# Optimization experiments

Hardware: AMD Instinct MI355X
Metric: run time of the kernel (lower is better)

Reference implementation:

```python
import jax, jax.numpy as jnp
import numpy as np

B, LQ, LK = 32, 2048, 2048
D_IN = 32   # vk_i_dim == q_i_dim == v_dim
D_KQ = 20   # kq_dim
EPS = 1e-5

def _layernorm(x, g, b):
    m = jnp.mean(x, axis=-1, keepdims=True)
    v = jnp.mean(jnp.square(x - m), axis=-1, keepdims=True)
    return (x - m) * jax.lax.rsqrt(v + EPS) * g + b

def setup_inputs() -> dict:
    key = jax.random.key(0)
    ks = jax.random.split(key, 8)
    s_in = 1.0 / np.sqrt(D_IN)
    return {
        "vals": jax.random.normal(ks[0], (B, LK, D_IN), jnp.float32),
        "keys": jax.random.normal(ks[1], (B, LK, D_IN), jnp.float32),
        "ques": jax.random.normal(ks[2], (B, LQ, D_IN), jnp.float32),
        "key_mask": jax.random.randint(ks[3], (B, LK), 0, 2) == 1,
        # Linear weights stored torch-style [out, in]; applied as x @ W.T
        "W_v": jax.random.uniform(ks[4], (D_IN, D_IN), jnp.float32, -s_in, s_in),
        "W_k": jax.random.uniform(ks[5], (D_KQ, D_IN), jnp.float32, -s_in, s_in),
        "W_q": jax.random.uniform(ks[6], (D_KQ, D_IN), jnp.float32, -s_in, s_in),
        "g_k": jnp.ones((D_KQ,), jnp.float32),
        "b_k": jnp.zeros((D_KQ,), jnp.float32),
        "g_q": jnp.ones((D_KQ,), jnp.float32),
        "b_q": jnp.zeros((D_KQ,), jnp.float32),
        "g_o": jnp.ones((D_IN,), jnp.float32),
        "b_o": jnp.zeros((D_IN,), jnp.float32),
    }

def reference(vals, keys, ques, key_mask, W_v, W_k, W_q, g_k, b_k, g_q, b_q, g_o, b_o):
    # v = linear_v(vals); k = LN(linear_k(keys)); q = LN(linear_q(ques))
    v = jnp.einsum('bkd,vd->bkv', vals, W_v)                    # [B,LK,32]
    k = _layernorm(jnp.einsum('bkd,cd->bkc', keys, W_k), g_k, b_k)  # [B,LK,20]
    q = _layernorm(jnp.einsum('bqd,cd->bqc', ques, W_q), g_q, b_q)  # [B,LQ,20]
    scale = jnp.asarray(D_KQ, jnp.float32) ** 0.5
    a = jnp.einsum('bqc,bkc->bqk', q, k) / scale                # [B,LQ,LK]
    a = jnp.where(key_mask[:, None, :], -jnp.inf, a)
    p = jax.nn.softmax(a, axis=-1)
    # dropout(p=0.1) in eval mode is identity
    o = jnp.einsum('bqk,bkv->bqv', p, v)                        # [B,LQ,32]
    return _layernorm(o + ques, g_o, b_o)
```

## Files before the change

kernel.cpp:

```cpp
#include <hip/hip_runtime.h>

#define NB   32
#define LQ   2048
#define LK   2048
#define EPSF 1e-5f
#define SCALE_L2E 0.32260327f
#define C_L2E     7.2134752f

#define MASK_I32  0
#define MASK_B8   1
#define MASK_BF16 2
#define MASK_F32  3

typedef __attribute__((ext_vector_type(8))) short  short8;
typedef __attribute__((ext_vector_type(4))) float  floatx4;

__device__ __forceinline__ unsigned short f2b(float f) {
    union { float f; unsigned int i; } c; c.f = f;
    unsigned int x = c.i;
    return (unsigned short)((x + 0x7FFFu + ((x >> 16) & 1u)) >> 16);
}

__device__ __forceinline__ int mask_nz(const void* m, int g, int enc) {
    switch (enc) {
        case MASK_B8:   return ((const unsigned char*)m)[g]  != 0;
        case MASK_BF16: return ((const unsigned short*)m)[g] != 0;
        case MASK_F32:  return ((const unsigned int*)m)[g]   != 0;
        default:        return ((const int*)m)[g]            != 0;
    }
}

__global__ __launch_bounds__(256) void proj_kv_kernel(
    const float4* __restrict__ vals,
    const float4* __restrict__ keys,
    const void*   __restrict__ key_mask,
    const float4* __restrict__ Wv,
    const float4* __restrict__ Wk,
    const float*  __restrict__ gk,
    const float*  __restrict__ bk,
    int*            __restrict__ counts,
    unsigned short* __restrict__ kbf,
    unsigned short* __restrict__ vTb)
{
    __shared__ float smem[1704];
    __shared__ int sc[3];
    float* sWv = smem;
    float* sWk = smem + 1024;
    float* sgk = smem + 1664;
    float* sbk = smem + 1684;
    const int tid = threadIdx.x;
    if (tid < 3) sc[tid] = 0;
    __syncthreads();

    ((float4*)sWv)[tid] = Wv[tid];
    if (tid < 160) ((float4*)sWk)[tid] = Wk[tid];
    if (tid < 20) sgk[tid] = gk[tid];
    if (tid >= 32 && tid < 52) sbk[tid - 32] = bk[tid - 32];
    {
        const unsigned char* mbytes = (const unsigned char*)key_mask;
        int l0 = 0, l1 = 0, l2 = 0;
        for (int i = tid; i < 1024; i += 256) {
            const unsigned char mb = mbytes[i];
            if ((i & 3) == 1 && mb == 0x3Fu) l0++;
            if ((i & 3) == 3 && mb == 0x3Fu) l1++;
            if ((i & 1) == 1 && mb == 0x01u) l2++;
        }
        if (l0) atomicAdd(&sc[0], l0);
        if (l1) atomicAdd(&sc[1], l1);
        if (l2) atomicAdd(&sc[2], l2);
    }
    __syncthreads();
    const int enc = sc[0] ? MASK_BF16 : (sc[1] ? MASK_F32 : (sc[2] ? MASK_B8 : MASK_I32));

    const int g = blockIdx.x * 256 + tid;
    const int b = g >> 11;
    const int lane = tid & 63;

    const int valid = mask_nz(key_mask, g, enc) ? 0 : 1;
    const unsigned long long mb = __ballot(valid);
    const int cnt = __popcll(mb);
    int base = 0;
    if (lane == 0) base = atomicAdd(&counts[b], cnt);
    base = __shfl(base, 0);
    const int slot = base + __popcll(mb & ((1ull << lane) - 1ull));

    float x[32];

    {
        const float4* kp = keys + (size_t)g * 8;
        #pragma unroll
        for (int t = 0; t < 8; ++t) {
            float4 u = kp[t];
            x[t*4+0] = u.x; x[t*4+1] = u.y; x[t*4+2] = u.z; x[t*4+3] = u.w;
        }
        const float4* wk4 = (const float4*)sWk;
        float kv[20];
        #pragma unroll
        for (int c = 0; c < 20; ++c) {
            float s = 0.f;
            #pragma unroll
            for (int i = 0; i < 8; ++i) {
                float4 ww = wk4[c * 8 + i];
                s = fmaf(x[i*4+0], ww.x, s); s = fmaf(x[i*4+1], ww.y, s);
                s = fmaf(x[i*4+2], ww.z, s); s = fmaf(x[i*4+3], ww.w, s);
            }
            kv[c] = s;
        }
        float m = 0.f;
        #pragma unroll
        for (int c = 0; c < 20; ++c) m += kv[c];
        m *= (1.f / 20.f);
        float v = 0.f;
        #pragma unroll
        for (int c = 0; c < 20; ++c) { float d = kv[c] - m; v += d * d; }
        v *= (1.f / 20.f);
        const float r = rsqrtf(v + EPSF);
        if (valid) {
            unsigned int u[16];
            #pragma unroll
            for (int j = 0; j < 10; ++j) {
                const float t0 = (kv[2*j]   - m) * r * sgk[2*j]   + sbk[2*j];
                const float t1 = (kv[2*j+1] - m) * r * sgk[2*j+1] + sbk[2*j+1];
                u[j] = (unsigned int)f2b(t0) | ((unsigned int)f2b(t1) << 16);
            }
            #pragma unroll
            for (int j = 10; j < 16; ++j) u[j] = 0u;
            uint4* dst = (uint4*)kbf + (size_t)(b * 2048 + slot) * 4;
            #pragma unroll
            for (int j = 0; j < 4; ++j)
                dst[j] = make_uint4(u[j*4], u[j*4+1], u[j*4+2], u[j*4+3]);
        }
    }

    {
        const float4* vp = vals + (size_t)g * 8;
        #pragma unroll
        for (int t = 0; t < 8; ++t) {
            float4 u = vp[t];
            x[t*4+0] = u.x; x[t*4+1] = u.y; x[t*4+2] = u.z; x[t*4+3] = u.w;
        }
        if (valid) {
            const float4* wv4 = (const float4*)sWv;
            #pragma unroll
            for (int o = 0; o < 32; ++o) {
                float s = 0.f;
                #pragma unroll
                for (int i = 0; i < 8; ++i) {
                    float4 ww = wv4[o * 8 + i];
                    s = fmaf(x[i*4+0], ww.x, s); s = fmaf(x[i*4+1], ww.y, s);
                    s = fmaf(x[i*4+2], ww.z, s); s = fmaf(x[i*4+3], ww.w, s);
                }
                vTb[((size_t)b * 32 + o) * 2048 + slot] = f2b(s);
            }
        }
    }
}

__global__ __launch_bounds__(256) void attn_kernel(
    const unsigned short* __restrict__ kbf,
    const unsigned short* __restrict__ vTb,
    const int*    __restrict__ counts,
    const float4* __restrict__ ques,
    const float4* __restrict__ Wq,
    const float*  __restrict__ gq,
    const float*  __restrict__ bq,
    const float*  __restrict__ go,
    const float*  __restrict__ bo,
    float* __restrict__ out)
{
    __shared__ uint4 smem4[2272];
    char*  smemB = (char*)smem4;
    float* smemF = (float*)smem4;

    const int tid  = threadIdx.x;
    const int w    = tid >> 6;
    const int lane = tid & 63;
    const int qcol = lane & 15;
    const int quad = lane >> 4;
    const int bb   = blockIdx.y;
    const int qbase = blockIdx.x * 64;

    if (tid < 160) ((float4*)smemF)[tid] = Wq[tid];
    if (tid >= 192 && tid < 212) smemF[640 + tid - 192] = gq[tid - 192];
    if (tid >= 224 && tid < 244) smemF[660 + tid - 224] = bq[tid - 224];
    __syncthreads();

    if (tid < 64) {
        const size_t grow = (size_t)bb * LQ + qbase + tid;
        float x[32];
        const float4* qp = ques + grow * 8;
        #pragma unroll
        for (int t = 0; t < 8; ++t) {
            float4 u = qp[t];
            x[t*4+0] = u.x; x[t*4+1] = u.y; x[t*4+2] = u.z; x[t*4+3] = u.w;
        }
        float qv[20];
        #pragma unroll
        for (int c = 0; c < 20; ++c) {
            float s = 0.f;
            #pragma unroll
            for (int i = 0; i < 32; ++i) s = fmaf(x[i], smemF[c*32 + i], s);
            qv[c] = s;
        }
        float m = 0.f;
        #pragma unroll
        for (int c = 0; c < 20; ++c) m += qv[c];
        m *= (1.f / 20.f);
        float v = 0.f;
        #pragma unroll
        for (int c = 0; c < 20; ++c) { float d = qv[c] - m; v += d * d; }
        v *= (1.f / 20.f);
        const float r = rsqrtf(v + EPSF);
        unsigned int u[16];
        #pragma unroll
        for (int j = 0; j < 10; ++j) {
            const float t0 = ((qv[2*j]   - m) * r * smemF[640+2*j]   + smemF[660+2*j])   * SCALE_L2E;
            const float t1 = ((qv[2*j+1] - m) * r * smemF[640+2*j+1] + smemF[660+2*j+1]) * SCALE_L2E;
            u[j] = (unsigned int)f2b(t0) | ((unsigned int)f2b(t1) << 16);
        }
        #pragma unroll
        for (int j = 10; j < 16; ++j) u[j] = 0u;
        uint4* dst = (uint4*)(smemB + 10240 + tid * 80);
        #pragma unroll
        for (int j = 0; j < 4; ++j)
            dst[j] = make_uint4(u[j*4], u[j*4+1], u[j*4+2], u[j*4+3]);
    }
    __syncthreads();

    const short8 qfrag = *(const short8*)(smemB + 10240 + (w*16 + qcol)*80 + quad*16);
    __syncthreads();

    const int nv = counts[bb];
    const int ntiles = (nv + 127) >> 7;
    const floatx4 cinit = { -C_L2E, -C_L2E, -C_L2E, -C_L2E };
    floatx4 oacc0 = {0.f, 0.f, 0.f, 0.f};
    floatx4 oacc1 = {0.f, 0.f, 0.f, 0.f};
    float lsum = 0.f;

    const unsigned short* kB = kbf + (size_t)bb * 2048 * 32;
    const unsigned short* vB = vTb + (size_t)bb * 32 * 2048;

    const int krow = tid >> 1, khalf = tid & 1;
    const int vd = tid >> 3,  vkg  = tid & 7;

    uint4 pk0, pk1, pv0, pv1;
    if (ntiles > 0) {
        const uint4* kp = (const uint4*)(kB + (size_t)krow * 32) + khalf * 2;
        pk0 = kp[0]; pk1 = kp[1];
        const uint4* vp = (const uint4*)(vB + (size_t)vd * 2048 + vkg * 16);
        pv0 = vp[0]; pv1 = vp[1];
    }

    char* pslab = smemB + 18944 + w*4352 + qcol*272;

    for (int t = 0; t < ntiles; ++t) {
        {
            uint4* kd = (uint4*)(smemB + krow*80 + khalf*32);
            kd[0] = pk0; kd[1] = pk1;
            uint4* vv = (uint4*)(smemB + 10240 + vd*272 + vkg*32);
            vv[0] = pv0; vv[1] = pv1;
        }
        __syncthreads();

        if (t + 1 < ntiles) {
            const int nb = (t + 1) << 7;
            const uint4* kp = (const uint4*)(kB + (size_t)(nb + krow) * 32) + khalf * 2;
            pk0 = kp[0]; pk1 = kp[1];
            const uint4* vp = (const uint4*)(vB + (size_t)vd * 2048 + nb + vkg * 16);
            pv0 = vp[0]; pv1 = vp[1];
        }

        const int base2 = t << 7;

        floatx4 sa[8];
        #pragma unroll
        for (int s = 0; s < 8; ++s) {
            const short8 ka = *(const short8*)(smemB + (s*16 + qcol)*80 + quad*16);
            sa[s] = __builtin_amdgcn_mfma_f32_16x16x32_bf16(ka, qfrag, cinit, 0, 0, 0);
        }

        #pragma unroll
        for (int s = 0; s < 8; ++s) {
            float p0, p1, p2, p3;
            const int kg = base2 + s*16 + quad*4;
            p0 = (kg     < nv) ? exp2f(sa[s][0]) : 0.f;
            p1 = (kg + 1 < nv) ? exp2f(sa[s][1]) : 0.f;
            p2 = (kg + 2 < nv) ? exp2f(sa[s][2]) : 0.f;
            p3 = (kg + 3 < nv) ? exp2f(sa[s][3]) : 0.f;
            lsum += (p0 + p1) + (p2 + p3);
            *(uint2*)(pslab + s*32 + quad*8) = make_uint2(
                (unsigned int)f2b(p0) | ((unsigned int)f2b(p1) << 16),
                (unsigned int)f2b(p2) | ((unsigned int)f2b(p3) << 16));
        }

        #pragma unroll
        for (int kk = 0; kk < 4; ++kk) {
            const short8 pf = *(const short8*)(pslab + kk*64 + quad*16);
            const short8 va = *(const short8*)(smemB + 10240 + qcol*272 + kk*64 + quad*16);
            const short8 vb = *(const short8*)(smemB + 10240 + (16+qcol)*272 + kk*64 + quad*16);
            oacc0 = __builtin_amdgcn_mfma_f32_16x16x32_bf16(va, pf, oacc0, 0, 0, 0);
            oacc1 = __builtin_amdgcn_mfma_f32_16x16x32_bf16(vb, pf, oacc1, 0, 0, 0);
        }
        __syncthreads();
    }

    {
        float* mrow = smemF + (w*16 + qcol) * 36;
        #pragma unroll
        for (int r = 0; r < 4; ++r) {
            mrow[quad*4 + r]      = oacc0[r];
            mrow[16 + quad*4 + r] = oacc1[r];
        }
        mrow[32 + quad] = lsum;
    }
    __syncthreads();

    if (tid < 64) {
        const float* mrow = smemF + tid * 36;
        const float ll = mrow[32] + mrow[33] + mrow[34] + mrow[35];
        const float inv = (ll > 0.f) ? 1.0f / ll : 0.f;
        const size_t grow = (size_t)bb * LQ + qbase + tid;
        float x[32];
        {
            const float4* qp = ques + grow * 8;
            #pragma unroll
            for (int t = 0; t < 8; ++t) {
                float4 u = qp[t];
                x[t*4+0] = u.x; x[t*4+1] = u.y; x[t*4+2] = u.z; x[t*4+3] = u.w;
            }
        }
        float m = 0.f;
        #pragma unroll
        for (int d = 0; d < 32; ++d) { x[d] = mrow[d] * inv + x[d]; m += x[d]; }
        m *= (1.f / 32.f);
        float v = 0.f;
        #pragma unroll
        for (int d = 0; d < 32; ++d) { float tt = x[d] - m; v += tt * tt; }
        v *= (1.f / 32.f);
        const float r = rsqrtf(v + EPSF);
        float y[32];
        #pragma unroll
        for (int d = 0; d < 32; ++d) y[d] = (x[d] - m) * r * go[d] + bo[d];
        float4* orow = (float4*)(out + grow * 32);
        #pragma unroll
        for (int j = 0; j < 8; ++j)
            orow[j] = make_float4(y[j*4], y[j*4+1], y[j*4+2], y[j*4+3]);
    }
}

extern "C" void kernel_launch(void* const* d_in, const int* in_sizes, int n_in,
                              void* d_out, int out_size, void* d_ws, size_t ws_size,
                              hipStream_t stream) {
    (void)in_sizes; (void)n_in; (void)out_size; (void)ws_size;
    const float4* vals = (const float4*)d_in[0];
    const float4* keys = (const float4*)d_in[1];
    const float4* ques = (const float4*)d_in[2];
    const void*   key_mask = d_in[3];
    const float4* Wv = (const float4*)d_in[4];
    const float4* Wk = (const float4*)d_in[5];
    const float4* Wq = (const float4*)d_in[6];
    const float* gk = (const float*)d_in[7];
    const float* bk = (const float*)d_in[8];
    const float* gq = (const float*)d_in[9];
    const float* bq = (const float*)d_in[10];
    const float* go = (const float*)d_in[11];
    const float* bo = (const float*)d_in[12];
    float* out = (float*)d_out;

    char* ws = (char*)d_ws;
    int*            counts = (int*)ws;
    unsigned short* kbf    = (unsigned short*)(ws + 512);
    unsigned short* vTb    = (unsigned short*)(ws + 512 + (size_t)NB*2048*32*2);

    hipMemsetAsync(counts, 0, NB * sizeof(int), stream);

    proj_kv_kernel<<<dim3((NB * LK) / 256), 256, 0, stream>>>(
        vals, keys, key_mask, Wv, Wk, gk, bk, counts, kbf, vTb);

    attn_kernel<<<dim3(LQ / 64, NB), 256, 0, stream>>>(
        kbf, vTb, counts, ques, Wq, gq, bq, go, bo, out);
}
```

Measured before the change: 161.2 us.

## Double attention block to 128 queries with 512 threads, fast exp and bf16 pack

The attention kernel now uses 512 threads and 128 queries per block, so every K/V tile staged in shared memory is reused by twice as many query rows. Each thread then loads one uint4 of K and one of V per tile, which halves the per-thread global traffic. Masking is skipped on full tiles, the raw hardware exp2 builtin is used, and bf16 packing goes through the HIP __float22bfloat162_rn intrinsic instead of manual rounding. The cost is more shared memory per block and half as many blocks, which may lower occupancy and parallelism.

```diff
diff --git a/kernel.cpp b/kernel.cpp
--- a/kernel.cpp
+++ b/kernel.cpp
@@ -1,4 +1,5 @@
 #include <hip/hip_runtime.h>
+#include <hip/hip_bf16.h>
 
 #define NB   32
 #define LQ   2048
@@ -19,6 +20,10 @@
     union { float f; unsigned int i; } c; c.f = f;
     unsigned int x = c.i;
     return (unsigned short)((x + 0x7FFFu + ((x >> 16) & 1u)) >> 16);
+}
+__device__ __forceinline__ unsigned int pkbf(float a, float b) {
+    __hip_bfloat162 h = __float22bfloat162_rn(make_float2(a, b));
+    union { __hip_bfloat162 h; unsigned int u; } c; c.h = h; return c.u;
 }
 
 __device__ __forceinline__ int mask_nz(const void* m, int g, int enc) {
@@ -121,7 +126,7 @@
             for (int j = 0; j < 10; ++j) {
                 const float t0 = (kv[2*j]   - m) * r * sgk[2*j]   + sbk[2*j];
                 const float t1 = (kv[2*j+1] - m) * r * sgk[2*j+1] + sbk[2*j+1];
-                u[j] = (unsigned int)f2b(t0) | ((unsigned int)f2b(t1) << 16);
+                u[j] = pkbf(t0, t1);
             }
             #pragma unroll
             for (int j = 10; j < 16; ++j) u[j] = 0u;
@@ -156,7 +161,7 @@
     }
 }
 
-__global__ __launch_bounds__(256) void attn_kernel(
+__global__ __launch_bounds__(512) void attn_kernel(
     const unsigned short* __restrict__ kbf,
     const unsigned short* __restrict__ vTb,
     const int*    __restrict__ counts,
@@ -168,7 +173,7 @@
     const float*  __restrict__ bo,
     float* __restrict__ out)
 {
-    __shared__ uint4 smem4[2272];
+    __shared__ uint4 smem4[3360];
     char*  smemB = (char*)smem4;
     float* smemF = (float*)smem4;
 
@@ -178,14 +183,14 @@
     const int qcol = lane & 15;
     const int quad = lane >> 4;
     const int bb   = blockIdx.y;
-    const int qbase = blockIdx.x * 64;
+    const int qbase = blockIdx.x * 128;
 
     if (tid < 160) ((float4*)smemF)[tid] = Wq[tid];
     if (tid >= 192 && tid < 212) smemF[640 + tid - 192] = gq[tid - 192];
     if (tid >= 224 && tid < 244) smemF[660 + tid - 224] = bq[tid - 224];
     __syncthreads();
 
-    if (tid < 64) {
+    if (tid < 128) {
         const size_t grow = (size_t)bb * LQ + qbase + tid;
         float x[32];
         const float4* qp = ques + grow * 8;
@@ -216,18 +221,18 @@
         for (int j = 0; j < 10; ++j) {
             const float t0 = ((qv[2*j]   - m) * r * smemF[640+2*j]   + smemF[660+2*j])   * SCALE_L2E;
             const float t1 = ((qv[2*j+1] - m) * r * smemF[640+2*j+1] + smemF[660+2*j+1]) * SCALE_L2E;
-            u[j] = (unsigned int)f2b(t0) | ((unsigned int)f2b(t1) << 16);
+            u[j] = pkbf(t0, t1);
         }
         #pragma unroll
         for (int j = 10; j < 16; ++j) u[j] = 0u;
-        uint4* dst = (uint4*)(smemB + 10240 + tid * 80);
+        uint4* dst = (uint4*)(smemB + 18944 + tid * 80);
         #pragma unroll
         for (int j = 0; j < 4; ++j)
             dst[j] = make_uint4(u[j*4], u[j*4+1], u[j*4+2], u[j*4+3]);
     }
     __syncthreads();
 
-    const short8 qfrag = *(const short8*)(smemB + 10240 + (w*16 + qcol)*80 + quad*16);
+    const short8 qfrag = *(const short8*)(smemB + 18944 + (w*16 + qcol)*80 + quad*16);
     __syncthreads();
 
     const int nv = counts[bb];
@@ -240,37 +245,30 @@
     const unsigned short* kB = kbf + (size_t)bb * 2048 * 32;
     const unsigned short* vB = vTb + (size_t)bb * 32 * 2048;
 
-    const int krow = tid >> 1, khalf = tid & 1;
-    const int vd = tid >> 3,  vkg  = tid & 7;
-
-    uint4 pk0, pk1, pv0, pv1;
+    const int krow = tid >> 2, kq = tid & 3;
+    const int vd   = tid >> 4, vkg = tid & 15;
+
+    uint4 pk, pv;
     if (ntiles > 0) {
-        const uint4* kp = (const uint4*)(kB + (size_t)krow * 32) + khalf * 2;
-        pk0 = kp[0]; pk1 = kp[1];
-        const uint4* vp = (const uint4*)(vB + (size_t)vd * 2048 + vkg * 16);
-        pv0 = vp[0]; pv1 = vp[1];
+        pk = *(const uint4*)(kB + (size_t)krow * 32 + kq * 8);
+        pv = *(const uint4*)(vB + (size_t)vd * 2048 + vkg * 8);
     }
 
     char* pslab = smemB + 18944 + w*4352 + qcol*272;
 
     for (int t = 0; t < ntiles; ++t) {
-        {
-            uint4* kd = (uint4*)(smemB + krow*80 + khalf*32);
-            kd[0] = pk0; kd[1] = pk1;
-            uint4* vv = (uint4*)(smemB + 10240 + vd*272 + vkg*32);
-            vv[0] = pv0; vv[1] = pv1;
-        }
+        *(uint4*)(smemB + krow*80 + kq*16)          = pk;
+        *(uint4*)(smemB + 10240 + vd*272 + vkg*16)  = pv;
         __syncthreads();
 
         if (t + 1 < ntiles) {
             const int nb = (t + 1) << 7;
-            const uint4* kp = (const uint4*)(kB + (size_t)(nb + krow) * 32) + khalf * 2;
-            pk0 = kp[0]; pk1 = kp[1];
-            const uint4* vp = (const uint4*)(vB + (size_t)vd * 2048 + nb + vkg * 16);
-            pv0 = vp[0]; pv1 = vp[1];
+            pk = *(const uint4*)(kB + (size_t)(nb + krow) * 32 + kq * 8);
+            pv = *(const uint4*)(vB + (size_t)vd * 2048 + nb + vkg * 8);
         }
 
         const int base2 = t << 7;
+        const bool full = (base2 + 128 <= nv);
 
         floatx4 sa[8];
         #pragma unroll
@@ -281,16 +279,19 @@
 
         #pragma unroll
         for (int s = 0; s < 8; ++s) {
-            float p0, p1, p2, p3;
-            const int kg = base2 + s*16 + quad*4;
-            p0 = (kg     < nv) ? exp2f(sa[s][0]) : 0.f;
-            p1 = (kg + 1 < nv) ? exp2f(sa[s][1]) : 0.f;
-            p2 = (kg + 2 < nv) ? exp2f(sa[s][2]) : 0.f;
-            p3 = (kg + 3 < nv) ? exp2f(sa[s][3]) : 0.f;
+            float p0 = __builtin_amdgcn_exp2f(sa[s][0]);
+            float p1 = __builtin_amdgcn_exp2f(sa[s][1]);
+            float p2 = __builtin_amdgcn_exp2f(sa[s][2]);
+            float p3 = __builtin_amdgcn_exp2f(sa[s][3]);
+            if (!full) {
+                const int kg = base2 + s*16 + quad*4;
+                p0 = (kg     < nv) ? p0 : 0.f;
+                p1 = (kg + 1 < nv) ? p1 : 0.f;
+                p2 = (kg + 2 < nv) ? p2 : 0.f;
+                p3 = (kg + 3 < nv) ? p3 : 0.f;
+            }
             lsum += (p0 + p1) + (p2 + p3);
-            *(uint2*)(pslab + s*32 + quad*8) = make_uint2(
-                (unsigned int)f2b(p0) | ((unsigned int)f2b(p1) << 16),
-                (unsigned int)f2b(p2) | ((unsigned int)f2b(p3) << 16));
+            *(uint2*)(pslab + s*32 + quad*8) = make_uint2(pkbf(p0, p1), pkbf(p2, p3));
         }
 
         #pragma unroll
@@ -315,7 +316,7 @@
     }
     __syncthreads();
 
-    if (tid < 64) {
+    if (tid < 128) {
         const float* mrow = smemF + tid * 36;
         const float ll = mrow[32] + mrow[33] + mrow[34] + mrow[35];
         const float inv = (ll > 0.f) ? 1.0f / ll : 0.f;
@@ -377,6 +378,6 @@
     proj_kv_kernel<<<dim3((NB * LK) / 256), 256, 0, stream>>>(
         vals, keys, key_mask, Wv, Wk, gk, bk, counts, kbf, vTb);
 
-    attn_kernel<<<dim3(LQ / 64, NB), 256, 0, stream>>>(
+    attn_kernel<<<dim3(LQ / 128, NB), 512, 0, stream>>>(
         kbf, vTb, counts, ques, Wq, gq, bq, go, bo, out);
 }
```

After: 139.6 us. 13.4% less time.
